# Kernel optimization log

Measured on AMD Instinct MI355X. Metric: run time of the kernel, lower is better.

## Reference

```python
import jax, jax.numpy as jnp
import numpy as np

INPUT_DIM, LATENT_DIM, HIDDEN_DIM, BATCH = 1024, 128, 1024, 32768


def setup_inputs() -> dict:
    key = jax.random.key(0)
    ks = jax.random.split(key, 12)
    s = 0.02
    x = (jax.random.uniform(ks[0], (BATCH, INPUT_DIM)) < 0.5).astype(jnp.float32)  # binary data
    eps = jax.random.normal(ks[1], (BATCH, LATENT_DIM), dtype=jnp.float32)
    return {
        "x": x,
        "eps": eps,
        "We1": jax.random.normal(ks[2], (INPUT_DIM, HIDDEN_DIM)) * s,
        "be1": jnp.zeros((HIDDEN_DIM,), jnp.float32),
        "Wmu": jax.random.normal(ks[3], (HIDDEN_DIM, LATENT_DIM)) * s,
        "bmu": jnp.zeros((LATENT_DIM,), jnp.float32),
        "Wls": jax.random.normal(ks[4], (HIDDEN_DIM, LATENT_DIM)) * s,
        "bls": jnp.zeros((LATENT_DIM,), jnp.float32),
        "Wd1": jax.random.normal(ks[5], (LATENT_DIM, HIDDEN_DIM)) * s,
        "bd1": jnp.zeros((HIDDEN_DIM,), jnp.float32),
        "Wd2": jax.random.normal(ks[6], (HIDDEN_DIM, INPUT_DIM)) * s,
        "bd2": jnp.zeros((INPUT_DIM,), jnp.float32),
    }


def reference(x, eps, We1, be1, Wmu, bmu, Wls, bls, Wd1, bd1, Wd2, bd2):
    # Encoder: one hidden ReLU layer, mu / logsigma heads
    h = jax.nn.relu(x @ We1 + be1)                      # [B, H]
    mu = h @ Wmu + bmu                                  # [B, L]
    logsigma = h @ Wls + bls                            # [B, L]
    # Reparameterization: z = sigma * eps + mu (vectorized diag(exp(logsigma)) @ eps)
    z = mu + jnp.exp(logsigma) * eps                    # [B, L]
    # Decoder: one hidden ReLU layer, sigmoid Bernoulli params
    hd = jax.nn.relu(z @ Wd1 + bd1)                     # [B, H]
    theta = jax.nn.sigmoid(hd @ Wd2 + bd2)              # [B, D]
    # Bernoulli log-likelihood: sum_j log(theta^x * (1-theta)^(1-x))
    log_px = jnp.sum(x * jnp.log(theta) + (1.0 - x) * jnp.log1p(-theta), axis=-1)  # [B]
    # KL(q||N(0,I)) = 0.5 * sum(sigma^2 + mu^2 - log(sigma^2) - 1)
    kl = 0.5 * jnp.sum(jnp.exp(2.0 * logsigma) + mu * mu - 2.0 * logsigma - 1.0, axis=-1)  # [B]
    return log_px - kl                                  # elbo_mc [B]
```

## Files before the change

kernel.cpp:

```cpp
#include <hip/hip_runtime.h>
#include <cstdint>
#include <cstddef>


typedef __bf16 bf16x8 __attribute__((ext_vector_type(8)));
typedef float f32x4 __attribute__((ext_vector_type(4)));

__device__ __forceinline__ unsigned short f32_to_bf16(float f) {
  unsigned int u = __float_as_uint(f);
  u += 0x7fffu + ((u >> 16) & 1u);
  return (unsigned short)(u >> 16);
}

struct TransJob { const float* in; unsigned short* out; int K, N, blkEnd; };

__global__ void prep_k(TransJob j0, TransJob j1, TransJob j2,
                       TransJob j3, TransJob j4,
                       const float* __restrict__ x,
                       unsigned short* __restrict__ xbit,
                       int n4, int castBlocks) {
  __shared__ float tile[32][33];
  int bid = blockIdx.x;
  int tx = threadIdx.x, ty = threadIdx.y;
  if (bid >= j4.blkEnd) {
    int tid = ty * 32 + tx;
    int stride = castBlocks * 256;
    for (int i = (bid - j4.blkEnd) * 256 + tid; i < n4; i += stride) {
      float4 v = reinterpret_cast<const float4*>(x)[i];
      unsigned int nib = (v.x != 0.f ? 1u : 0u) | (v.y != 0.f ? 2u : 0u) |
                         (v.z != 0.f ? 4u : 0u) | (v.w != 0.f ? 8u : 0u);
      unsigned int n1 = __shfl_down(nib, 1, 64);
      unsigned int n2 = __shfl_down(nib, 2, 64);
      unsigned int n3 = __shfl_down(nib, 3, 64);
      if ((tid & 3) == 0)
        xbit[i >> 2] = (unsigned short)(nib | (n1 << 4) | (n2 << 8) | (n3 << 12));
    }
    return;
  }
  TransJob j; int base;
  if (bid < j0.blkEnd)      { j = j0; base = 0; }
  else if (bid < j1.blkEnd) { j = j1; base = j0.blkEnd; }
  else if (bid < j2.blkEnd) { j = j2; base = j1.blkEnd; }
  else if (bid < j3.blkEnd) { j = j3; base = j2.blkEnd; }
  else                      { j = j4; base = j3.blkEnd; }
  int local = bid - base;
  int gxN = j.N >> 5;
  int n0 = (local % gxN) * 32, k0 = (local / gxN) * 32;
#pragma unroll
  for (int r = 0; r < 32; r += 8)
    tile[ty + r][tx] = j.in[(size_t)(k0 + ty + r) * j.N + n0 + tx];
  __syncthreads();
#pragma unroll
  for (int r = 0; r < 32; r += 8)
    j.out[(size_t)(n0 + ty + r) * j.K + k0 + tx] = f32_to_bf16(tile[tx][ty + r]);
}

__device__ __forceinline__ void gl_lds16(const unsigned short* g, unsigned short* l) {
  __builtin_amdgcn_global_load_lds(
      (__attribute__((address_space(1))) void*)g,
      (__attribute__((address_space(3))) void*)l, 16, 0, 0);
}

template <int EPI, int TAG, int ABIT>
__global__ __launch_bounds__(512, 2) void gemm256(
    const unsigned short* __restrict__ A, const unsigned short* __restrict__ BT,
    int gx, int N, int K,
    const float* __restrict__ bias0,
    unsigned short* __restrict__ outb, float* __restrict__ outf,
    const unsigned short* __restrict__ xbit) {
  __shared__ __align__(16) unsigned short smem[65536];

  const int tid = threadIdx.x;
  const int lane = tid & 63;
  const int wave = tid >> 6;
  const int wr = wave >> 2;
  const int wc = wave & 3;
  const int lm = lane & 15, lq = lane >> 4;
  const int sw = lm & 7;

  const int bid = blockIdx.x;
  const int xcd = bid & 7;
  const int t8 = bid >> 3;
  const int m0 = (xcd + 8 * (t8 / gx)) * 256;
  const int n0 = (t8 % gx) * 256;
  const int NT = K >> 6;

  unsigned short* const smemp = smem;
  auto Abuf = [&](int b) -> unsigned short* {
    return ABIT ? smemp : smemp + b * 32768;
  };
  auto Bbuf = [&](int b) -> unsigned short* {
    return ABIT ? smemp + 16384 + b * 16384 : smemp + b * 32768 + 16384;
  };

  const unsigned short* gpA[2];
  const unsigned short* gpB[2];
  int loA[2], loB[2], xaddr[2];
#pragma unroll
  for (int r = 0; r < 2; ++r) {
    int c = tid + 512 * r, rl = c >> 3, q8 = c & 7;
    int rowA = (rl & 63) + ((rl >> 6) << 7);
    int rowB = (rl & 31) + ((rl >> 5) << 6);
    int qgA = q8 ^ (rowA & 7);
    gpA[r] = A + (size_t)(m0 + rowA) * K + qgA * 8;
    gpB[r] = BT + (size_t)(n0 + rowB) * K + (q8 ^ (rowB & 7)) * 8;
    loA[r] = rowA * 64 + q8 * 8;
    loB[r] = rowB * 64 + q8 * 8;
    xaddr[r] = rowA * 128 + qgA;
  }

  auto stage = [&](int kind, int buf, int kt) {
#pragma unroll
    for (int r = 0; r < 2; ++r) {
      if (kind == 0)      { if (!ABIT) gl_lds16(gpA[r] + kt * 64,          Abuf(buf) + loA[r]); }
      else if (kind == 3) { if (!ABIT) gl_lds16(gpA[r] + 64 * K + kt * 64, Abuf(buf) + loA[r] + 4096); }
      else if (kind == 1) gl_lds16(gpB[r] + kt * 64,          Bbuf(buf) + loB[r]);
      else                gl_lds16(gpB[r] + 32 * K + kt * 64, Bbuf(buf) + loB[r] + 2048);
    }
  };

  auto expandA = [&](int t) {
    const unsigned char* xsb = reinterpret_cast<const unsigned char*>(smemp + 49152);
    unsigned short* As = smemp;
#pragma unroll
    for (int r = 0; r < 2; ++r) {
#pragma unroll
      for (int h = 0; h < 2; ++h) {
        unsigned int b = xsb[xaddr[r] + h * 8192 + 8 * t];
        unsigned int o0 = ((b & 1u)        ? 0x3F80u : 0u) | ((b & 2u)   ? 0x3F800000u : 0u);
        unsigned int o1 = (((b >> 2) & 1u) ? 0x3F80u : 0u) | ((b & 8u)   ? 0x3F800000u : 0u);
        unsigned int o2 = (((b >> 4) & 1u) ? 0x3F80u : 0u) | ((b & 32u)  ? 0x3F800000u : 0u);
        unsigned int o3 = (((b >> 6) & 1u) ? 0x3F80u : 0u) | ((b & 128u) ? 0x3F800000u : 0u);
        *reinterpret_cast<uint4*>(As + loA[r] + h * 4096) = make_uint4(o0, o1, o2, o3);
      }
    }
  };

  if (ABIT) {
    const unsigned short* xp = xbit + (size_t)m0 * 64;
    unsigned short* xs = smemp + 49152;
#pragma unroll
    for (int i = 0; i < 4; ++i)
      gl_lds16(xp + (tid + 512 * i) * 8, xs + (tid + 512 * i) * 8);
    stage(1, 0, 0); stage(2, 0, 0);
    stage(1, 1, 1); stage(2, 1, 1);
    asm volatile("s_waitcnt vmcnt(8)" ::: "memory");
    expandA(0);
    asm volatile("s_waitcnt vmcnt(4) lgkmcnt(0)" ::: "memory");
    __builtin_amdgcn_s_barrier();
  } else {
    stage(0, 0, 0); stage(1, 0, 0); stage(2, 0, 0); stage(3, 0, 0);
    stage(0, 1, 1); stage(1, 1, 1); stage(2, 1, 1);
    asm volatile("s_waitcnt vmcnt(6)" ::: "memory");
    __builtin_amdgcn_s_barrier();
  }

  f32x4 acc[8][4] = {};

  const int aRow = (wr * 128 + lm) * 64;
  const int bRow = (wc * 64 + lm) * 64;
  const int c0 = ((0 | lq) ^ sw) * 8;
  const int c1 = ((4 | lq) ^ sw) * 8;

  for (int t = 0; t < NT; ++t) {
    const int b = t & 1;
    const unsigned short* Ab = Abuf(b);
    const unsigned short* Bb = Bbuf(b);
    bf16x8 af[4][2], bf1[2][2], bf2[2][2];

#pragma unroll
    for (int i = 0; i < 4; ++i) {
      af[i][0] = *reinterpret_cast<const bf16x8*>(Ab + aRow + i * 1024 + c0);
      af[i][1] = *reinterpret_cast<const bf16x8*>(Ab + aRow + i * 1024 + c1);
    }
#pragma unroll
    for (int j = 0; j < 2; ++j) {
      bf1[j][0] = *reinterpret_cast<const bf16x8*>(Bb + bRow + j * 1024 + c0);
      bf1[j][1] = *reinterpret_cast<const bf16x8*>(Bb + bRow + j * 1024 + c1);
    }
    if (!ABIT && t + 1 < NT) stage(3, (t + 1) & 1, t + 1);
    __builtin_amdgcn_s_barrier();
    asm volatile("s_waitcnt lgkmcnt(0)" ::: "memory");
    __builtin_amdgcn_sched_barrier(0);
    __builtin_amdgcn_s_setprio(1);
#pragma unroll
    for (int s = 0; s < 2; ++s)
#pragma unroll
      for (int i = 0; i < 4; ++i)
#pragma unroll
        for (int j = 0; j < 2; ++j)
          acc[i][j] = __builtin_amdgcn_mfma_f32_16x16x32_bf16(af[i][s], bf1[j][s], acc[i][j], 0, 0, 0);
    __builtin_amdgcn_s_setprio(0);
    __builtin_amdgcn_s_barrier();

#pragma unroll
    for (int j = 0; j < 2; ++j) {
      bf2[j][0] = *reinterpret_cast<const bf16x8*>(Bb + bRow + (j + 2) * 1024 + c0);
      bf2[j][1] = *reinterpret_cast<const bf16x8*>(Bb + bRow + (j + 2) * 1024 + c1);
    }
    if (t + 2 < NT) stage(ABIT ? 1 : 0, b, t + 2);
    __builtin_amdgcn_s_barrier();
    asm volatile("s_waitcnt lgkmcnt(0)" ::: "memory");
    __builtin_amdgcn_sched_barrier(0);
    __builtin_amdgcn_s_setprio(1);
#pragma unroll
    for (int s = 0; s < 2; ++s)
#pragma unroll
      for (int i = 0; i < 4; ++i)
#pragma unroll
        for (int j = 0; j < 2; ++j)
          acc[i][j + 2] = __builtin_amdgcn_mfma_f32_16x16x32_bf16(af[i][s], bf2[j][s], acc[i][j + 2], 0, 0, 0);
    __builtin_amdgcn_s_setprio(0);
    __builtin_amdgcn_s_barrier();

#pragma unroll
    for (int i = 0; i < 4; ++i) {
      af[i][0] = *reinterpret_cast<const bf16x8*>(Ab + aRow + (64 + i * 16) * 64 + c0);
      af[i][1] = *reinterpret_cast<const bf16x8*>(Ab + aRow + (64 + i * 16) * 64 + c1);
    }
    if (t + 2 < NT) stage(ABIT ? 2 : 1, b, t + 2);
    __builtin_amdgcn_s_barrier();
    asm volatile("s_waitcnt lgkmcnt(0)" ::: "memory");
    __builtin_amdgcn_sched_barrier(0);
    __builtin_amdgcn_s_setprio(1);
#pragma unroll
    for (int s = 0; s < 2; ++s)
#pragma unroll
      for (int i = 0; i < 4; ++i)
#pragma unroll
        for (int j = 0; j < 2; ++j)
          acc[i + 4][j] = __builtin_amdgcn_mfma_f32_16x16x32_bf16(af[i][s], bf1[j][s], acc[i + 4][j], 0, 0, 0);
    __builtin_amdgcn_s_setprio(0);
    __builtin_amdgcn_s_barrier();

    if (ABIT) { if (t + 1 < NT) expandA(t + 1); }
    else      { if (t + 2 < NT) stage(2, b, t + 2); }
    __builtin_amdgcn_s_barrier();
    __builtin_amdgcn_s_setprio(1);
#pragma unroll
    for (int s = 0; s < 2; ++s)
#pragma unroll
      for (int i = 0; i < 4; ++i)
#pragma unroll
        for (int j = 0; j < 2; ++j)
          acc[i + 4][j + 2] = __builtin_amdgcn_mfma_f32_16x16x32_bf16(af[i][s], bf2[j][s], acc[i + 4][j + 2], 0, 0, 0);
    __builtin_amdgcn_s_setprio(0);
    if (ABIT) {
      if (t + 2 < NT) { asm volatile("s_waitcnt vmcnt(4) lgkmcnt(0)" ::: "memory"); }
      else            { asm volatile("s_waitcnt vmcnt(0) lgkmcnt(0)" ::: "memory"); }
    } else {
      if (t + 2 < NT)      { asm volatile("s_waitcnt vmcnt(6)" ::: "memory"); }
      else if (t + 1 < NT) { asm volatile("s_waitcnt vmcnt(0)" ::: "memory"); }
    }
    __builtin_amdgcn_s_barrier();
  }

  if (EPI == 0) {
#pragma unroll
    for (int i = 0; i < 8; ++i)
#pragma unroll
      for (int j = 0; j < 4; ++j) {
        int col = n0 + wc * 64 + j * 16 + lm;
        float bias = bias0[col];
#pragma unroll
        for (int r = 0; r < 4; ++r) {
          int row = m0 + wr * 128 + i * 16 + lq * 4 + r;
          float v = acc[i][j][r] + bias;
          outb[(size_t)row * N + col] = f32_to_bf16(fmaxf(v, 0.f));
        }
      }
  } else {
    const int wpr = N >> 4;
#pragma unroll
    for (int i = 0; i < 8; ++i) {
      float rs[4] = {0.f, 0.f, 0.f, 0.f};
#pragma unroll
      for (int j = 0; j < 4; ++j) {
        int col = n0 + wc * 64 + j * 16 + lm;
        float bias = bias0[col];
        int w16 = (col >> 4);
#pragma unroll
        for (int r = 0; r < 4; ++r) {
          int row = m0 + wr * 128 + i * 16 + lq * 4 + r;
          float l = acc[i][j][r] + bias;
          unsigned short mask = xbit[(size_t)row * wpr + w16];
          float tt = ((mask >> lm) & 1) ? -l : l;
          float sp = fmaxf(tt, 0.f) + __logf(1.f + __expf(-fabsf(tt)));
          rs[r] -= sp;
        }
      }
#pragma unroll
      for (int off = 1; off < 16; off <<= 1)
#pragma unroll
        for (int r = 0; r < 4; ++r) rs[r] += __shfl_xor(rs[r], off, 64);
      if (lm == 0) {
#pragma unroll
        for (int r = 0; r < 4; ++r)
          atomicAdd(&outf[m0 + wr * 128 + i * 16 + lq * 4 + r], rs[r]);
      }
    }
  }
}

__global__ __launch_bounds__(256, 1) void latent_fused(
    const unsigned short* A,
    const unsigned short* __restrict__ BT,
    const unsigned short* __restrict__ WD1,
    const float* __restrict__ bmu, const float* __restrict__ bls,
    const float* __restrict__ bd1,
    const float* __restrict__ eps,
    unsigned short* hd,
    float* __restrict__ out) {
  __shared__ __align__(16) unsigned short smem[65536];
  unsigned short* As0 = smem;
  unsigned short* As1 = smem + 8192;
  unsigned short* Bs0 = smem + 16384;
  unsigned short* Bs1 = smem + 32768;
  unsigned short* zs  = smem + 49152;
  unsigned short* Bs2 = smem;

  const int K = 1024;
  const int tid = threadIdx.x;
  const int lane = tid & 63;
  const int wave = tid >> 6;
  const int m0 = blockIdx.x * 128;
  const int lm = lane & 15, lq = lane >> 4;
  const int sw = lm & 7;

  const unsigned short* agp[4];
  const unsigned short* bgp[8];
#pragma unroll
  for (int r = 0; r < 4; ++r) {
    int c = tid + 256 * r;
    int row = c >> 3, q = (c & 7) ^ (row & 7);
    agp[r] = A + (size_t)(m0 + row) * K + q * 8;
  }
#pragma unroll
  for (int r = 0; r < 8; ++r) {
    int c = tid + 256 * r;
    int row = c >> 3, q = (c & 7) ^ (row & 7);
    bgp[r] = BT + (size_t)row * K + q * 8;
  }

  auto stage1 = [&](int buf, int kt) {
    unsigned short* Ad = buf ? As1 : As0;
    unsigned short* Bd = buf ? Bs1 : Bs0;
#pragma unroll
    for (int r = 0; r < 4; ++r) gl_lds16(agp[r] + kt, Ad + (tid + 256 * r) * 8);
#pragma unroll
    for (int r = 0; r < 8; ++r) gl_lds16(bgp[r] + kt, Bd + (tid + 256 * r) * 8);
  };

  f32x4 acc[2][16] = {};

  stage1(0, 0);
  __syncthreads();

  for (int t = 0; t < 16; ++t) {
    const int cur = t & 1;
    if (t + 1 < 16) stage1(cur ^ 1, (t + 1) * 64);
    const unsigned short* Ab = cur ? As1 : As0;
    const unsigned short* Bb = cur ? Bs1 : Bs0;
#pragma unroll
    for (int s = 0; s < 2; ++s) {
      const int so = ((s << 2) | lq) ^ sw;
      bf16x8 af[2];
#pragma unroll
      for (int i = 0; i < 2; ++i)
        af[i] = *reinterpret_cast<const bf16x8*>(Ab + (wave * 32 + i * 16 + lm) * 64 + so * 8);
#pragma unroll
      for (int j = 0; j < 16; ++j) {
        bf16x8 b = *reinterpret_cast<const bf16x8*>(Bb + (j * 16 + lm) * 64 + so * 8);
        acc[0][j] = __builtin_amdgcn_mfma_f32_16x16x32_bf16(af[0], b, acc[0][j], 0, 0, 0);
        acc[1][j] = __builtin_amdgcn_mfma_f32_16x16x32_bf16(af[1], b, acc[1][j], 0, 0, 0);
      }
    }
    __syncthreads();
  }

  auto stage2 = [&](int nt) {
#pragma unroll
    for (int ri = 0; ri < 16; ++ri) {
      int c = tid + 256 * ri;
      int row = c >> 4, slot = c & 15;
      int gc = slot ^ (row & 7);
      gl_lds16(WD1 + (size_t)(nt * 256 + row) * 128 + gc * 8, Bs2 + c * 8);
    }
  };
  stage2(0);

#pragma unroll
  for (int i = 0; i < 2; ++i) {
    float kl[4] = {0.f, 0.f, 0.f, 0.f};
#pragma unroll
    for (int j = 0; j < 8; ++j) {
      int dim = j * 16 + lm;
      float bm = bmu[dim], bl = bls[dim];
#pragma unroll
      for (int r = 0; r < 4; ++r) {
        int rowl = wave * 32 + i * 16 + lq * 4 + r;
        float mu = acc[i][j][r] + bm;
        float ls = acc[i][j + 8][r] + bl;
        float e = eps[(size_t)(m0 + rowl) * 128 + dim];
        float zv = fmaf(__expf(ls), e, mu);
        int chunk = (dim >> 3);
        int slot = chunk ^ (rowl & 7);
        zs[rowl * 128 + slot * 8 + (lm & 7)] = f32_to_bf16(zv);
        kl[r] += 0.5f * (__expf(2.f * ls) + mu * mu - 2.f * ls - 1.f);
      }
    }
#pragma unroll
    for (int off = 1; off < 16; off <<= 1)
#pragma unroll
      for (int r = 0; r < 4; ++r) kl[r] += __shfl_xor(kl[r], off, 64);
    if (lm == 0) {
#pragma unroll
      for (int r = 0; r < 4; ++r)
        out[m0 + wave * 32 + i * 16 + lq * 4 + r] = -kl[r];
    }
  }

  for (int nt = 0; nt < 4; ++nt) {
    asm volatile("s_waitcnt vmcnt(0)" ::: "memory");
    __syncthreads();
    f32x4 acc2[2][16] = {};
#pragma unroll
    for (int ks = 0; ks < 4; ++ks) {
      const int cks = (ks * 4 + lq) ^ (lm & 7);
      bf16x8 a0 = *reinterpret_cast<const bf16x8*>(zs + (wave * 32 + lm) * 128 + cks * 8);
      bf16x8 a1 = *reinterpret_cast<const bf16x8*>(zs + (wave * 32 + 16 + lm) * 128 + cks * 8);
#pragma unroll
      for (int j = 0; j < 16; ++j) {
        bf16x8 b = *reinterpret_cast<const bf16x8*>(Bs2 + (j * 16 + lm) * 128 + cks * 8);
        acc2[0][j] = __builtin_amdgcn_mfma_f32_16x16x32_bf16(a0, b, acc2[0][j], 0, 0, 0);
        acc2[1][j] = __builtin_amdgcn_mfma_f32_16x16x32_bf16(a1, b, acc2[1][j], 0, 0, 0);
      }
    }
    __syncthreads();
    if (nt + 1 < 4) stage2(nt + 1);
#pragma unroll
    for (int i = 0; i < 2; ++i)
#pragma unroll
      for (int j = 0; j < 16; ++j) {
        int col = nt * 256 + j * 16 + lm;
        float bias = bd1[col];
#pragma unroll
        for (int r = 0; r < 4; ++r) {
          int row = m0 + wave * 32 + i * 16 + lq * 4 + r;
          float v = acc2[i][j][r] + bias;
          hd[(size_t)row * 1024 + col] = f32_to_bf16(fmaxf(v, 0.f));
        }
      }
  }
}

extern "C" void kernel_launch(void* const* d_in, const int* in_sizes, int n_in,
                              void* d_out, int out_size, void* d_ws, size_t ws_size,
                              hipStream_t stream) {
  const float* x   = (const float*)d_in[0];
  const float* eps = (const float*)d_in[1];
  const float* We1 = (const float*)d_in[2];
  const float* be1 = (const float*)d_in[3];
  const float* Wmu = (const float*)d_in[4];
  const float* bmu = (const float*)d_in[5];
  const float* Wls = (const float*)d_in[6];
  const float* bls = (const float*)d_in[7];
  const float* Wd1 = (const float*)d_in[8];
  const float* bd1 = (const float*)d_in[9];
  const float* Wd2 = (const float*)d_in[10];
  const float* bd2 = (const float*)d_in[11];
  float* out = (float*)d_out;

  const int B = 32768, D = 1024, H = 1024, L = 128;

  char* ws = (char*)d_ws;
  size_t off = 0;
  auto alloc = [&](size_t bytes) {
    void* p = ws + off;
    off += (bytes + 255) & ~(size_t)255;
    return p;
  };
  unsigned short* xbit = (unsigned short*)alloc((size_t)B * D / 8);
  unsigned short* w1t  = (unsigned short*)alloc((size_t)H * D * 2);
  unsigned short* w2t  = (unsigned short*)alloc((size_t)256 * H * 2);
  unsigned short* wd1t = (unsigned short*)alloc((size_t)H * L * 2);
  unsigned short* wd2t = (unsigned short*)alloc((size_t)D * H * 2);
  unsigned short* h    = (unsigned short*)alloc((size_t)B * H * 2);
  unsigned short* hd   = h;

  TransJob j0{We1, w1t, D, H, 1024};
  TransJob j1{Wmu, w2t, H, L, 1152};
  TransJob j2{Wls, w2t + 128 * H, H, L, 1280};
  TransJob j3{Wd1, wd1t, L, H, 1408};
  TransJob j4{Wd2, wd2t, H, D, 2432};
  prep_k<<<2432 + 2048, dim3(32, 8), 0, stream>>>(
      j0, j1, j2, j3, j4, x, xbit, B * D / 4, 2048);

  gemm256<0, 1, 1><<<512, 512, 0, stream>>>(
      nullptr, w1t, 4, H, D, be1, h, nullptr, xbit);
  latent_fused<<<B / 128, 256, 0, stream>>>(
      h, w2t, wd1t, bmu, bls, bd1, eps, hd, out);
  gemm256<2, 4, 0><<<512, 512, 0, stream>>>(
      hd, wd2t, 4, D, H, bd2, nullptr, out, xbit);

  (void)in_sizes; (void)n_in; (void)out_size; (void)ws_size;
}
```

Baseline: 438.5 us.

## Shrink latent_fused tiles to 64 rows to allow two blocks per CU

```diff
diff --git a/kernel.cpp b/kernel.cpp
--- a/kernel.cpp
+++ b/kernel.cpp
@@ -302,7 +302,7 @@
   }
 }
 
-__global__ __launch_bounds__(256, 1) void latent_fused(
+__global__ __launch_bounds__(256, 2) void latent_fused(
     const unsigned short* A,
     const unsigned short* __restrict__ BT,
     const unsigned short* __restrict__ WD1,
@@ -311,86 +311,74 @@
     const float* __restrict__ eps,
     unsigned short* hd,
     float* __restrict__ out) {
-  __shared__ __align__(16) unsigned short smem[65536];
+  __shared__ __align__(16) unsigned short smem[28672];
   unsigned short* As0 = smem;
-  unsigned short* As1 = smem + 8192;
-  unsigned short* Bs0 = smem + 16384;
-  unsigned short* Bs1 = smem + 32768;
-  unsigned short* zs  = smem + 49152;
+  unsigned short* As1 = smem + 2048;
+  unsigned short* Bs0 = smem + 4096;
+  unsigned short* Bs1 = smem + 12288;
+  unsigned short* zs  = smem + 20480;
   unsigned short* Bs2 = smem;
 
   const int K = 1024;
   const int tid = threadIdx.x;
   const int lane = tid & 63;
   const int wave = tid >> 6;
-  const int m0 = blockIdx.x * 128;
+  const int m0 = blockIdx.x * 64;
   const int lm = lane & 15, lq = lane >> 4;
-  const int sw = lm & 7;
-
-  const unsigned short* agp[4];
-  const unsigned short* bgp[8];
+  const int sw2 = (lm >> 1) & 3;
+
+  const unsigned short* agp;
+  const unsigned short* bgp[4];
+  {
+    int row = tid >> 2, q = tid & 3;
+    agp = A + (size_t)(m0 + row) * K + (q ^ ((row >> 1) & 3)) * 8;
+  }
 #pragma unroll
   for (int r = 0; r < 4; ++r) {
     int c = tid + 256 * r;
-    int row = c >> 3, q = (c & 7) ^ (row & 7);
-    agp[r] = A + (size_t)(m0 + row) * K + q * 8;
-  }
-#pragma unroll
-  for (int r = 0; r < 8; ++r) {
-    int c = tid + 256 * r;
-    int row = c >> 3, q = (c & 7) ^ (row & 7);
-    bgp[r] = BT + (size_t)row * K + q * 8;
+    int row = c >> 2, q = c & 3;
+    bgp[r] = BT + (size_t)row * K + (q ^ ((row >> 1) & 3)) * 8;
   }
 
   auto stage1 = [&](int buf, int kt) {
-    unsigned short* Ad = buf ? As1 : As0;
+    gl_lds16(agp + kt, (buf ? As1 : As0) + tid * 8);
     unsigned short* Bd = buf ? Bs1 : Bs0;
 #pragma unroll
-    for (int r = 0; r < 4; ++r) gl_lds16(agp[r] + kt, Ad + (tid + 256 * r) * 8);
-#pragma unroll
-    for (int r = 0; r < 8; ++r) gl_lds16(bgp[r] + kt, Bd + (tid + 256 * r) * 8);
-  };
-
-  f32x4 acc[2][16] = {};
+    for (int r = 0; r < 4; ++r) gl_lds16(bgp[r] + kt, Bd + (tid + 256 * r) * 8);
+  };
+
+  f32x4 acc[16] = {};
 
   stage1(0, 0);
   __syncthreads();
 
-  for (int t = 0; t < 16; ++t) {
+  const int aOff = (wave * 16 + lm) * 32 + (lq ^ sw2) * 8;
+  for (int t = 0; t < 32; ++t) {
     const int cur = t & 1;
-    if (t + 1 < 16) stage1(cur ^ 1, (t + 1) * 64);
+    if (t + 1 < 32) stage1(cur ^ 1, (t + 1) * 32);
     const unsigned short* Ab = cur ? As1 : As0;
     const unsigned short* Bb = cur ? Bs1 : Bs0;
-#pragma unroll
-    for (int s = 0; s < 2; ++s) {
-      const int so = ((s << 2) | lq) ^ sw;
-      bf16x8 af[2];
-#pragma unroll
-      for (int i = 0; i < 2; ++i)
-        af[i] = *reinterpret_cast<const bf16x8*>(Ab + (wave * 32 + i * 16 + lm) * 64 + so * 8);
-#pragma unroll
-      for (int j = 0; j < 16; ++j) {
-        bf16x8 b = *reinterpret_cast<const bf16x8*>(Bb + (j * 16 + lm) * 64 + so * 8);
-        acc[0][j] = __builtin_amdgcn_mfma_f32_16x16x32_bf16(af[0], b, acc[0][j], 0, 0, 0);
-        acc[1][j] = __builtin_amdgcn_mfma_f32_16x16x32_bf16(af[1], b, acc[1][j], 0, 0, 0);
-      }
+    bf16x8 af = *reinterpret_cast<const bf16x8*>(Ab + aOff);
+#pragma unroll
+    for (int j = 0; j < 16; ++j) {
+      bf16x8 b = *reinterpret_cast<const bf16x8*>(Bb + (j * 16 + lm) * 32 + (lq ^ sw2) * 8);
+      acc[j] = __builtin_amdgcn_mfma_f32_16x16x32_bf16(af, b, acc[j], 0, 0, 0);
     }
     __syncthreads();
   }
 
-  auto stage2 = [&](int nt) {
-#pragma unroll
-    for (int ri = 0; ri < 16; ++ri) {
+  auto stage2 = [&](int hh) {
+#pragma unroll
+    for (int ri = 0; ri < 8; ++ri) {
       int c = tid + 256 * ri;
       int row = c >> 4, slot = c & 15;
       int gc = slot ^ (row & 7);
-      gl_lds16(WD1 + (size_t)(nt * 256 + row) * 128 + gc * 8, Bs2 + c * 8);
+      gl_lds16(WD1 + (size_t)(hh * 128 + row) * 128 + gc * 8, Bs2 + c * 8);
     }
   };
   stage2(0);
 
-#pragma unroll
-  for (int i = 0; i < 2; ++i) {
+  {
     float kl[4] = {0.f, 0.f, 0.f, 0.f};
 #pragma unroll
     for (int j = 0; j < 8; ++j) {
@@ -398,9 +386,9 @@
       float bm = bmu[dim], bl = bls[dim];
 #pragma unroll
       for (int r = 0; r < 4; ++r) {
-        int rowl = wave * 32 + i * 16 + lq * 4 + r;
-        float mu = acc[i][j][r] + bm;
-        float ls = acc[i][j + 8][r] + bl;
+        int rowl = wave * 16 + lq * 4 + r;
+        float mu = acc[j][r] + bm;
+        float ls = acc[j + 8][r] + bl;
         float e = eps[(size_t)(m0 + rowl) * 128 + dim];
         float zv = fmaf(__expf(ls), e, mu);
         int chunk = (dim >> 3);
@@ -416,41 +404,37 @@
     if (lm == 0) {
 #pragma unroll
       for (int r = 0; r < 4; ++r)
-        out[m0 + wave * 32 + i * 16 + lq * 4 + r] = -kl[r];
-    }
-  }
-
-  for (int nt = 0; nt < 4; ++nt) {
+        out[m0 + wave * 16 + lq * 4 + r] = -kl[r];
+    }
+  }
+
+  for (int hh = 0; hh < 8; ++hh) {
     asm volatile("s_waitcnt vmcnt(0)" ::: "memory");
     __syncthreads();
-    f32x4 acc2[2][16] = {};
+    f32x4 acc2[8] = {};
 #pragma unroll
     for (int ks = 0; ks < 4; ++ks) {
       const int cks = (ks * 4 + lq) ^ (lm & 7);
-      bf16x8 a0 = *reinterpret_cast<const bf16x8*>(zs + (wave * 32 + lm) * 128 + cks * 8);
-      bf16x8 a1 = *reinterpret_cast<const bf16x8*>(zs + (wave * 32 + 16 + lm) * 128 + cks * 8);
-#pragma unroll
-      for (int j = 0; j < 16; ++j) {
+      bf16x8 a0 = *reinterpret_cast<const bf16x8*>(zs + (wave * 16 + lm) * 128 + cks * 8);
+#pragma unroll
+      for (int j = 0; j < 8; ++j) {
         bf16x8 b = *reinterpret_cast<const bf16x8*>(Bs2 + (j * 16 + lm) * 128 + cks * 8);
-        acc2[0][j] = __builtin_amdgcn_mfma_f32_16x16x32_bf16(a0, b, acc2[0][j], 0, 0, 0);
-        acc2[1][j] = __builtin_amdgcn_mfma_f32_16x16x32_bf16(a1, b, acc2[1][j], 0, 0, 0);
+        acc2[j] = __builtin_amdgcn_mfma_f32_16x16x32_bf16(a0, b, acc2[j], 0, 0, 0);
       }
     }
     __syncthreads();
-    if (nt + 1 < 4) stage2(nt + 1);
-#pragma unroll
-    for (int i = 0; i < 2; ++i)
-#pragma unroll
-      for (int j = 0; j < 16; ++j) {
-        int col = nt * 256 + j * 16 + lm;
-        float bias = bd1[col];
-#pragma unroll
-        for (int r = 0; r < 4; ++r) {
-          int row = m0 + wave * 32 + i * 16 + lq * 4 + r;
-          float v = acc2[i][j][r] + bias;
-          hd[(size_t)row * 1024 + col] = f32_to_bf16(fmaxf(v, 0.f));
-        }
-      }
+    if (hh + 1 < 8) stage2(hh + 1);
+#pragma unroll
+    for (int j = 0; j < 8; ++j) {
+      int col = hh * 128 + j * 16 + lm;
+      float bias = bd1[col];
+#pragma unroll
+      for (int r = 0; r < 4; ++r) {
+        int row = m0 + wave * 16 + lq * 4 + r;
+        float v = acc2[j][r] + bias;
+        hd[(size_t)row * 1024 + col] = f32_to_bf16(fmaxf(v, 0.f));
+      }
+    }
   }
 }
 
@@ -498,7 +482,7 @@
 
   gemm256<0, 1, 1><<<512, 512, 0, stream>>>(
       nullptr, w1t, 4, H, D, be1, h, nullptr, xbit);
-  latent_fused<<<B / 128, 256, 0, stream>>>(
+  latent_fused<<<B / 64, 256, 0, stream>>>(
       h, w2t, wd1t, bmu, bls, bd1, eps, hd, out);
   gemm256<2, 4, 0><<<512, 512, 0, stream>>>(
       hd, wd2t, 4, D, H, bd2, nullptr, out, xbit);
```

New measurement: 430.2 us, median of 2. About the same (-1.9%).
